# Optimization experiments

Hardware: AMD Instinct MI355X
Metric: run time of the kernel (lower is better)

## Reference

```python
import jax, jax.numpy as jnp
import numpy as np

NODES = 1024
IN_F = 512
OUT_F = 256
BATCH = 32768


def setup_inputs() -> dict:
    key = jax.random.key(0)
    k1, k2, k3 = jax.random.split(key, 3)
    bound = 1.0 / np.sqrt(NODES)  # torch Linear default init range
    x = jax.random.normal(k1, (BATCH, IN_F), dtype=jnp.float32)
    W = jax.random.uniform(k2, (NODES, NODES), dtype=jnp.float32, minval=-bound, maxval=bound)
    b = jax.random.uniform(k3, (NODES,), dtype=jnp.float32, minval=-bound, maxval=bound)
    return {"x": x, "W": W, "b": b}


def reference(x, W, b):
    # state = [x, zeros]; next = W @ state + b; output = next[out_nodes]
    # out_nodes = [nodes-1-i for i in range(out_features)]  (reversed tail)
    out_idx = jnp.arange(NODES - 1, NODES - 1 - OUT_F, -1)  # [OUT_F]
    W_sel = W[out_idx, :IN_F]                               # [OUT_F, IN_F]
    b_sel = b[out_idx]                                      # [OUT_F]
    return x @ W_sel.T + b_sel                              # [BATCH, OUT_F]
```

## Files before the change

### kernel.cpp

```cpp
#include <hip/hip_runtime.h>
#include <hip/hip_bf16.h>


#define M_TOT 32768
#define K_TOT 512
#define N_TOT 256
#define W_LD  1024

#define BM 128
#define BN 256
#define BK 64
#define NTH 512
#define KSTEPS 8

#define LDS_ABYTES (BM * BK * 2)
#define LDS_BUF    (LDS_ABYTES + BN * BK * 2)

typedef __bf16 bf16x8 __attribute__((ext_vector_type(8)));
typedef float  f32x4  __attribute__((ext_vector_type(4)));

static __device__ __forceinline__ bf16x8 cvt8(f32x4 a, f32x4 b) {
    bf16x8 r;
    r[0] = (__bf16)a[0]; r[1] = (__bf16)a[1]; r[2] = (__bf16)a[2]; r[3] = (__bf16)a[3];
    r[4] = (__bf16)b[0]; r[5] = (__bf16)b[1]; r[6] = (__bf16)b[2]; r[7] = (__bf16)b[3];
    return r;
}

__global__ __launch_bounds__(NTH, 2)
void ng_gemm(const float* __restrict__ x, const float* __restrict__ W,
             const float* __restrict__ bias, float* __restrict__ out)
{
    __shared__ __align__(16) unsigned char lds[2 * LDS_BUF];

    const int tid  = threadIdx.x;
    const int lane = tid & 63;
    const int wid  = tid >> 6;
    const int wr   = wid >> 2;
    const int wc   = wid & 3;
    const long mBase = (long)blockIdx.x * BM;

    const int srow = tid >> 3;
    const int skg  = tid & 7;
    const float* srcA = x + (mBase + srow) * K_TOT + skg * 8;
    const float* srcB = W + (long)(1023 - srow) * W_LD + skg * 8;
    const int swz0 = srow * (BK * 2) + ((skg * 16) ^ ((srow & 7) << 4));

    int rdA[2][4], rdB[2][4];
#pragma unroll
    for (int ks = 0; ks < 2; ++ks) {
        const int col = ks * 64 + (lane >> 4) * 16;
#pragma unroll
        for (int i = 0; i < 4; ++i) {
            const int ra = wr * 64 + i * 16 + (lane & 15);
            const int rb = wc * 64 + i * 16 + (lane & 15);
            rdA[ks][i] = ra * (BK * 2) + (col ^ ((ra & 7) << 4));
            rdB[ks][i] = LDS_ABYTES + rb * (BK * 2) + (col ^ ((rb & 7) << 4));
        }
    }

    f32x4 acc[4][4];
#pragma unroll
    for (int mi = 0; mi < 4; ++mi)
#pragma unroll
        for (int ni = 0; ni < 4; ++ni)
            acc[mi][ni] = (f32x4){0.f, 0.f, 0.f, 0.f};

    f32x4 rgA[2][2], rgB[4][2];

#define LOADT(kt_) do {                                                   \
        const float* pa_ = srcA + (kt_) * BK;                             \
        rgA[0][0] = *(const f32x4*)(pa_);                                 \
        rgA[0][1] = *(const f32x4*)(pa_ + 4);                             \
        rgA[1][0] = *(const f32x4*)(pa_ + 64 * K_TOT);                    \
        rgA[1][1] = *(const f32x4*)(pa_ + 64 * K_TOT + 4);                \
        const float* pb_ = srcB + (kt_) * BK;                             \
        rgB[0][0] = *(const f32x4*)(pb_);                                 \
        rgB[0][1] = *(const f32x4*)(pb_ + 4);                             \
        rgB[1][0] = *(const f32x4*)(pb_ - 64 * W_LD);                     \
        rgB[1][1] = *(const f32x4*)(pb_ - 64 * W_LD + 4);                 \
        rgB[2][0] = *(const f32x4*)(pb_ - 128 * W_LD);                    \
        rgB[2][1] = *(const f32x4*)(pb_ - 128 * W_LD + 4);                \
        rgB[3][0] = *(const f32x4*)(pb_ - 192 * W_LD);                    \
        rgB[3][1] = *(const f32x4*)(pb_ - 192 * W_LD + 4);                \
    } while (0)

#define WRITET(base_) do {                                                              \
        *(bf16x8*)(lds + (base_) + swz0)                         = cvt8(rgA[0][0], rgA[0][1]); \
        *(bf16x8*)(lds + (base_) + swz0 + 64 * 128)              = cvt8(rgA[1][0], rgA[1][1]); \
        *(bf16x8*)(lds + (base_) + LDS_ABYTES + swz0)            = cvt8(rgB[0][0], rgB[0][1]); \
        *(bf16x8*)(lds + (base_) + LDS_ABYTES + swz0 + 1 * 8192) = cvt8(rgB[1][0], rgB[1][1]); \
        *(bf16x8*)(lds + (base_) + LDS_ABYTES + swz0 + 2 * 8192) = cvt8(rgB[2][0], rgB[2][1]); \
        *(bf16x8*)(lds + (base_) + LDS_ABYTES + swz0 + 3 * 8192) = cvt8(rgB[3][0], rgB[3][1]); \
    } while (0)

#define COMPUTET(base_) do {                                                    \
        _Pragma("unroll")                                                       \
        for (int ks_ = 0; ks_ < 2; ++ks_) {                                     \
            bf16x8 af_[4], bf_[4];                                              \
            _Pragma("unroll")                                                   \
            for (int i_ = 0; i_ < 4; ++i_) {                                    \
                af_[i_] = *(const bf16x8*)(lds + (base_) + rdA[ks_][i_]);       \
                bf_[i_] = *(const bf16x8*)(lds + (base_) + rdB[ks_][i_]);       \
            }                                                                   \
            _Pragma("unroll")                                                   \
            for (int mi_ = 0; mi_ < 4; ++mi_)                                   \
                _Pragma("unroll")                                               \
                for (int ni_ = 0; ni_ < 4; ++ni_)                               \
                    acc[mi_][ni_] = __builtin_amdgcn_mfma_f32_16x16x32_bf16(    \
                        af_[mi_], bf_[ni_], acc[mi_][ni_], 0, 0, 0);            \
        }                                                                       \
    } while (0)

    LOADT(0);
    WRITET(0);
    __syncthreads();

#pragma unroll
    for (int t = 0; t < KSTEPS; ++t) {
        const int cur = (t & 1) * LDS_BUF;
        const int nxt = LDS_BUF - cur;
        if (t + 1 < KSTEPS) LOADT(t + 1);
        COMPUTET(cur);
        if (t + 1 < KSTEPS) WRITET(nxt);
        __syncthreads();
    }

    const int cRow = wr * 64 + (lane >> 4) * 4;
    const int cCol = wc * 64 + (lane & 15);
#pragma unroll
    for (int ni = 0; ni < 4; ++ni) {
        const int gn = cCol + ni * 16;
        const float bv = bias[1023 - gn];
#pragma unroll
        for (int mi = 0; mi < 4; ++mi) {
            float* dst = out + (mBase + cRow + mi * 16) * (long)N_TOT + gn;
#pragma unroll
            for (int i = 0; i < 4; ++i)
                dst[(long)i * N_TOT] = acc[mi][ni][i] + bv;
        }
    }
#undef LOADT
#undef WRITET
#undef COMPUTET
}

extern "C" void kernel_launch(void* const* d_in, const int* in_sizes, int n_in,
                              void* d_out, int out_size, void* d_ws, size_t ws_size,
                              hipStream_t stream) {
    const float* x = (const float*)d_in[0];
    const float* W = (const float*)d_in[1];
    const float* b = (const float*)d_in[2];
    float* out = (float*)d_out;
    ng_gemm<<<dim3(M_TOT / BM), dim3(NTH), 0, stream>>>(x, W, b, out);
}
```

Measured before the change: 114.0 us.

## Pre-pack W into swizzled bf16 image and stream it via global_load_lds

A small prep kernel converts the selected, reversed rows of W into a bf16 image laid out exactly as the LDS swizzle expects, stored in the workspace. The GEMM then copies B tiles straight into LDS with global_load_lds, skipping the register round trip and the per-block fp32-to-bf16 conversion. The M tile is halved to 64 and occupancy raised to 4 blocks per CU, giving 512 blocks. The cost is an extra kernel launch, and each block now does less work while still loading the full B tile.

```diff
diff --git a/kernel.cpp b/kernel.cpp
--- a/kernel.cpp
+++ b/kernel.cpp
@@ -7,14 +7,14 @@
 #define N_TOT 256
 #define W_LD  1024
 
-#define BM 128
-#define BN 256
+#define BM 64
 #define BK 64
 #define NTH 512
 #define KSTEPS 8
 
-#define LDS_ABYTES (BM * BK * 2)
-#define LDS_BUF    (LDS_ABYTES + BN * BK * 2)
+#define A_BYTES (BM * BK * 2)
+#define B_BYTES (N_TOT * BK * 2)
+#define LDS_BUF (A_BYTES + B_BYTES)
 
 typedef __bf16 bf16x8 __attribute__((ext_vector_type(8)));
 typedef float  f32x4  __attribute__((ext_vector_type(4)));
@@ -26,8 +26,25 @@
     return r;
 }
 
-__global__ __launch_bounds__(NTH, 2)
-void ng_gemm(const float* __restrict__ x, const float* __restrict__ W,
+__global__ __launch_bounds__(256)
+void ng_prep(const float* __restrict__ W, unsigned char* __restrict__ img)
+{
+    const int id = blockIdx.x * 256 + threadIdx.x;
+    const int kt = id >> 11;
+    const int r  = (id >> 3) & 255;
+    const int c  = id & 7;
+    const float* src = W + (long)(1023 - r) * W_LD + kt * 64 + c * 8;
+    f32x4 a = *(const f32x4*)src;
+    f32x4 b = *(const f32x4*)(src + 4);
+    *(bf16x8*)(img + kt * B_BYTES + r * 128 + ((c * 16) ^ ((r & 7) << 4))) = cvt8(a, b);
+}
+
+#define GLL16(gp_, lp_) __builtin_amdgcn_global_load_lds(                     \
+        (const __attribute__((address_space(1))) void*)(gp_),                 \
+        (__attribute__((address_space(3))) void*)(lp_), 16, 0, 0)
+
+__global__ __launch_bounds__(NTH, 4)
+void ng_gemm(const float* __restrict__ x, const unsigned char* __restrict__ wimg,
              const float* __restrict__ bias, float* __restrict__ out)
 {
     __shared__ __align__(16) unsigned char lds[2 * LDS_BUF];
@@ -35,112 +52,112 @@
     const int tid  = threadIdx.x;
     const int lane = tid & 63;
     const int wid  = tid >> 6;
-    const int wr   = wid >> 2;
-    const int wc   = wid & 3;
+    const int wrow = wid >> 2;
+    const int wcol = wid & 3;
     const long mBase = (long)blockIdx.x * BM;
 
-    const int srow = tid >> 3;
+    const int arow = tid >> 3;
     const int skg  = tid & 7;
-    const float* srcA = x + (mBase + srow) * K_TOT + skg * 8;
-    const float* srcB = W + (long)(1023 - srow) * W_LD + skg * 8;
-    const int swz0 = srow * (BK * 2) + ((skg * 16) ^ ((srow & 7) << 4));
+    const float* srcA = x + (mBase + arow) * K_TOT + skg * 8;
+    const int swzA = arow * 128 + ((skg * 16) ^ ((arow & 7) << 4));
 
-    int rdA[2][4], rdB[2][4];
+    int rdA[2][2], rdB[2][4];
 #pragma unroll
     for (int ks = 0; ks < 2; ++ks) {
         const int col = ks * 64 + (lane >> 4) * 16;
 #pragma unroll
-        for (int i = 0; i < 4; ++i) {
-            const int ra = wr * 64 + i * 16 + (lane & 15);
-            const int rb = wc * 64 + i * 16 + (lane & 15);
-            rdA[ks][i] = ra * (BK * 2) + (col ^ ((ra & 7) << 4));
-            rdB[ks][i] = LDS_ABYTES + rb * (BK * 2) + (col ^ ((rb & 7) << 4));
+        for (int i = 0; i < 2; ++i) {
+            const int ra = wrow * 32 + i * 16 + (lane & 15);
+            rdA[ks][i] = ra * 128 + (col ^ ((ra & 7) << 4));
+        }
+#pragma unroll
+        for (int j = 0; j < 4; ++j) {
+            const int rb = wcol * 64 + j * 16 + (lane & 15);
+            rdB[ks][j] = A_BYTES + rb * 128 + (col ^ ((rb & 7) << 4));
         }
     }
 
-    f32x4 acc[4][4];
+    f32x4 acc[2][4];
 #pragma unroll
-    for (int mi = 0; mi < 4; ++mi)
+    for (int mi = 0; mi < 2; ++mi)
 #pragma unroll
         for (int ni = 0; ni < 4; ++ni)
             acc[mi][ni] = (f32x4){0.f, 0.f, 0.f, 0.f};
 
-    f32x4 rgA[2][2], rgB[4][2];
+    f32x4 rgA0, rgA1;
 
-#define LOADT(kt_) do {                                                   \
-        const float* pa_ = srcA + (kt_) * BK;                             \
-        rgA[0][0] = *(const f32x4*)(pa_);                                 \
-        rgA[0][1] = *(const f32x4*)(pa_ + 4);                             \
-        rgA[1][0] = *(const f32x4*)(pa_ + 64 * K_TOT);                    \
-        rgA[1][1] = *(const f32x4*)(pa_ + 64 * K_TOT + 4);                \
-        const float* pb_ = srcB + (kt_) * BK;                             \
-        rgB[0][0] = *(const f32x4*)(pb_);                                 \
-        rgB[0][1] = *(const f32x4*)(pb_ + 4);                             \
-        rgB[1][0] = *(const f32x4*)(pb_ - 64 * W_LD);                     \
-        rgB[1][1] = *(const f32x4*)(pb_ - 64 * W_LD + 4);                 \
-        rgB[2][0] = *(const f32x4*)(pb_ - 128 * W_LD);                    \
-        rgB[2][1] = *(const f32x4*)(pb_ - 128 * W_LD + 4);                \
-        rgB[3][0] = *(const f32x4*)(pb_ - 192 * W_LD);                    \
-        rgB[3][1] = *(const f32x4*)(pb_ - 192 * W_LD + 4);                \
+#define STAGEB(kt_, base_) do {                                               \
+        const unsigned char* s_ = wimg + (kt_) * B_BYTES;                     \
+        _Pragma("unroll")                                                     \
+        for (int c_ = 0; c_ < 4; ++c_)                                        \
+            GLL16(s_ + c_ * 8192 + tid * 16,                                  \
+                  lds + (base_) + A_BYTES + c_ * 8192 + wid * 1024);          \
     } while (0)
 
-#define WRITET(base_) do {                                                              \
-        *(bf16x8*)(lds + (base_) + swz0)                         = cvt8(rgA[0][0], rgA[0][1]); \
-        *(bf16x8*)(lds + (base_) + swz0 + 64 * 128)              = cvt8(rgA[1][0], rgA[1][1]); \
-        *(bf16x8*)(lds + (base_) + LDS_ABYTES + swz0)            = cvt8(rgB[0][0], rgB[0][1]); \
-        *(bf16x8*)(lds + (base_) + LDS_ABYTES + swz0 + 1 * 8192) = cvt8(rgB[1][0], rgB[1][1]); \
-        *(bf16x8*)(lds + (base_) + LDS_ABYTES + swz0 + 2 * 8192) = cvt8(rgB[2][0], rgB[2][1]); \
-        *(bf16x8*)(lds + (base_) + LDS_ABYTES + swz0 + 3 * 8192) = cvt8(rgB[3][0], rgB[3][1]); \
+#define LOADA(kt_) do {                                                       \
+        const float* p_ = srcA + (kt_) * BK;                                  \
+        rgA0 = *(const f32x4*)(p_);                                           \
+        rgA1 = *(const f32x4*)(p_ + 4);                                       \
     } while (0)
 
-#define COMPUTET(base_) do {                                                    \
-        _Pragma("unroll")                                                       \
-        for (int ks_ = 0; ks_ < 2; ++ks_) {                                     \
-            bf16x8 af_[4], bf_[4];                                              \
-            _Pragma("unroll")                                                   \
-            for (int i_ = 0; i_ < 4; ++i_) {                                    \
-                af_[i_] = *(const bf16x8*)(lds + (base_) + rdA[ks_][i_]);       \
-                bf_[i_] = *(const bf16x8*)(lds + (base_) + rdB[ks_][i_]);       \
-            }                                                                   \
-            _Pragma("unroll")                                                   \
-            for (int mi_ = 0; mi_ < 4; ++mi_)                                   \
-                _Pragma("unroll")                                               \
-                for (int ni_ = 0; ni_ < 4; ++ni_)                               \
-                    acc[mi_][ni_] = __builtin_amdgcn_mfma_f32_16x16x32_bf16(    \
-                        af_[mi_], bf_[ni_], acc[mi_][ni_], 0, 0, 0);            \
-        }                                                                       \
+#define WRITEA(base_) do {                                                    \
+        *(bf16x8*)(lds + (base_) + swzA) = cvt8(rgA0, rgA1);                  \
     } while (0)
 
-    LOADT(0);
-    WRITET(0);
+#define COMPUTET(base_) do {                                                  \
+        _Pragma("unroll")                                                     \
+        for (int ks_ = 0; ks_ < 2; ++ks_) {                                   \
+            bf16x8 af_[2], bf_[4];                                            \
+            _Pragma("unroll")                                                 \
+            for (int i_ = 0; i_ < 2; ++i_)                                    \
+                af_[i_] = *(const bf16x8*)(lds + (base_) + rdA[ks_][i_]);     \
+            _Pragma("unroll")                                                 \
+            for (int j_ = 0; j_ < 4; ++j_)                                    \
+                bf_[j_] = *(const bf16x8*)(lds + (base_) + rdB[ks_][j_]);     \
+            _Pragma("unroll")                                                 \
+            for (int mi_ = 0; mi_ < 2; ++mi_)                                 \
+                _Pragma("unroll")                                             \
+                for (int ni_ = 0; ni_ < 4; ++ni_)                             \
+                    acc[mi_][ni_] = __builtin_amdgcn_mfma_f32_16x16x32_bf16(  \
+                        af_[mi_], bf_[ni_], acc[mi_][ni_], 0, 0, 0);          \
+        }                                                                     \
+    } while (0)
+
+    STAGEB(0, 0);
+    LOADA(0);
+    WRITEA(0);
     __syncthreads();
 
 #pragma unroll
     for (int t = 0; t < KSTEPS; ++t) {
         const int cur = (t & 1) * LDS_BUF;
         const int nxt = LDS_BUF - cur;
-        if (t + 1 < KSTEPS) LOADT(t + 1);
+        if (t + 1 < KSTEPS) {
+            STAGEB(t + 1, nxt);
+            LOADA(t + 1);
+        }
         COMPUTET(cur);
-        if (t + 1 < KSTEPS) WRITET(nxt);
+        if (t + 1 < KSTEPS) WRITEA(nxt);
         __syncthreads();
     }
 
-    const int cRow = wr * 64 + (lane >> 4) * 4;
-    const int cCol = wc * 64 + (lane & 15);
+    const int cRow = wrow * 32 + (lane >> 4) * 4;
+    const int cCol = wcol * 64 + (lane & 15);
 #pragma unroll
     for (int ni = 0; ni < 4; ++ni) {
         const int gn = cCol + ni * 16;
         const float bv = bias[1023 - gn];
 #pragma unroll
-        for (int mi = 0; mi < 4; ++mi) {
+        for (int mi = 0; mi < 2; ++mi) {
             float* dst = out + (mBase + cRow + mi * 16) * (long)N_TOT + gn;
 #pragma unroll
             for (int i = 0; i < 4; ++i)
                 dst[(long)i * N_TOT] = acc[mi][ni][i] + bv;
         }
     }
-#undef LOADT
-#undef WRITET
+#undef STAGEB
+#undef LOADA
+#undef WRITEA
 #undef COMPUTET
 }
 
@@ -151,5 +168,8 @@
     const float* W = (const float*)d_in[1];
     const float* b = (const float*)d_in[2];
     float* out = (float*)d_out;
-    ng_gemm<<<dim3(M_TOT / BM), dim3(NTH), 0, stream>>>(x, W, b, out);
+    unsigned char* img = (unsigned char*)d_ws;
+
+    ng_prep<<<dim3(64), dim3(256), 0, stream>>>(W, img);
+    ng_gemm<<<dim3(M_TOT / BM), dim3(NTH), 0, stream>>>(x, img, b, out);
 }
```

After: 113.4 us. About the same (-0.6%).
